# Optimization experiments

Measured on AMD Instinct MI355X. Metric: run time of the kernel, lower is better.

Reference implementation:

```python
import jax, jax.numpy as jnp
import numpy as np

# Mamba-1.4B-like dims
BATCH, SEQ, HID = 1, 2048, 2048
INTER, STATE, DT_RANK, KCONV = 4096, 16, 128, 4


def setup_inputs() -> dict:
    key = jax.random.key(0)
    ks = jax.random.split(key, 8)
    f = jnp.float32
    return {
        "input_states": jax.random.normal(ks[0], (BATCH, SEQ, HID), f),
        "in_proj_w": jax.random.normal(ks[1], (HID, 2 * INTER), f) * (HID ** -0.5),
        "conv_w": jax.random.normal(ks[2], (INTER, 1, KCONV), f) * (KCONV ** -0.5),  # (O, I/groups=1, K) depthwise
        "conv_b": jnp.zeros((INTER,), f),
        "x_proj_w": jax.random.normal(ks[3], (INTER, DT_RANK + 2 * STATE), f) * (INTER ** -0.5),
        "dt_proj_w": jax.random.normal(ks[4], (DT_RANK, INTER), f) * (DT_RANK ** -0.5),
        "dt_proj_b": jax.random.normal(ks[5], (INTER,), f) * 0.1,
        "A_log": jnp.log(jnp.broadcast_to(jnp.arange(1, STATE + 1, dtype=f), (INTER, STATE))),
        "D": jnp.ones((INTER,), f),
        "out_proj_w": jax.random.normal(ks[6], (INTER, HID), f) * (INTER ** -0.5),
    }


def _mamba_forward(input_states, in_proj_w, conv_w, conv_b, x_proj_w,
                   dt_proj_w, dt_proj_b, A_log, D, out_proj_w):
    Bsz, L, _ = input_states.shape
    Idim, _, K = conv_w.shape
    N = A_log.shape[1]
    R = dt_proj_w.shape[0]

    proj = input_states @ in_proj_w                       # (B, L, 2I)
    hidden, gate = jnp.split(proj, 2, axis=-1)            # each (B, L, I)

    # depthwise causal conv over sequence (pad K-1, keep first L outputs)
    xc = jnp.swapaxes(hidden, 1, 2)                       # (B, I, L)
    xc = jax.lax.conv_general_dilated(
        xc, conv_w, window_strides=(1,), padding=((K - 1, K - 1),),
        feature_group_count=Idim)
    xc = xc[:, :, :L] + conv_b[None, :, None]
    u = jax.nn.silu(jnp.swapaxes(xc, 1, 2))               # (B, L, I)

    # input-dependent SSM params
    ssm_in = u @ x_proj_w                                 # (B, L, R + 2N)
    dt_in, Bc, Cc = jnp.split(ssm_in, [R, R + N], axis=-1)
    dt = jax.nn.softplus(dt_in @ dt_proj_w + dt_proj_b)   # (B, L, I)
    A = -jnp.exp(A_log)                                   # (I, N)

    def step(state, xs):
        dt_t, B_t, C_t, u_t = xs                          # (B,I) (B,N) (B,N) (B,I)
        dA = jnp.exp(dt_t[:, :, None] * A[None])          # (B, I, N)
        state = state * dA + (dt_t * u_t)[:, :, None] * B_t[:, None, :]
        y_t = jnp.einsum('bin,bn->bi', state, C_t)
        return state, y_t

    xs = (jnp.swapaxes(dt, 0, 1), jnp.swapaxes(Bc, 0, 1),
          jnp.swapaxes(Cc, 0, 1), jnp.swapaxes(u, 0, 1))
    state0 = jnp.zeros((Bsz, Idim, N), dt.dtype)
    _, ys = jax.lax.scan(step, state0, xs)                # (L, B, I)
    y = jnp.swapaxes(ys, 0, 1)                            # (B, L, I)

    y = (y + u * D) * jax.nn.silu(gate)
    return y @ out_proj_w                                 # (B, L, H)


def reference(input_states, in_proj_w, conv_w, conv_b, x_proj_w,
              dt_proj_w, dt_proj_b, A_log, D, out_proj_w):
    return _mamba_forward(input_states, in_proj_w, conv_w, conv_b, x_proj_w,
                          dt_proj_w, dt_proj_b, A_log, D, out_proj_w)
```

## Files before the change

kernel.cpp:

```cpp
#include <hip/hip_runtime.h>
#include <stdint.h>

#define LSEQ 2048
#define HID  2048
#define IDIM 4096
#define NSTATE 16
#define RRANK 128
#define GDIM 160

#define GCHUNK 64
#define TCHUNK (LSEQ / GCHUNK)

typedef _Float16 f16x8 __attribute__((ext_vector_type(8)));
typedef _Float16 f16x2 __attribute__((ext_vector_type(2)));
typedef float f32x4 __attribute__((ext_vector_type(4)));

#define GLOAD_LDS16(g, l) __builtin_amdgcn_global_load_lds( \
    (const __attribute__((address_space(1))) void*)(g),     \
    (__attribute__((address_space(3))) void*)(l), 16, 0, 0)

__device__ __forceinline__ float softplus_f(float x) {
    if (x > 20.f) return x;
    return log1pf(__expf(x));
}
__device__ __forceinline__ float silu_f(float x) {
    return x / (1.f + __expf(-x));
}

__device__ __forceinline__ void transpose_tile(const float* __restrict__ in,
                                               _Float16* __restrict__ out,
                                               int R, int C, int tr, int tc,
                                               _Float16 (*tile)[66]) {
    const int c0 = tc * 64, r0 = tr * 64;
    const int t = threadIdx.x;
    const int tx = t & 15, ty = t >> 4;
    const int ox = t & 7, oy = t >> 3;
    const bool full = (c0 + 64 <= C) && (r0 + 64 <= R);
    if (full) {
        #pragma unroll
        for (int j = 0; j < 4; ++j) {
            int r = ty + j * 16;
            float4 v = *(const float4*)(in + (long)(r0 + r) * C + c0 + tx * 4);
            tile[r][tx * 4 + 0] = (_Float16)v.x;
            tile[r][tx * 4 + 1] = (_Float16)v.y;
            tile[r][tx * 4 + 2] = (_Float16)v.z;
            tile[r][tx * 4 + 3] = (_Float16)v.w;
        }
        __syncthreads();
        #pragma unroll
        for (int j = 0; j < 2; ++j) {
            int c = oy + j * 32;
            f16x8 v;
            #pragma unroll
            for (int e = 0; e < 8; ++e) v[e] = tile[ox * 8 + e][c];
            *(f16x8*)(out + (long)(c0 + c) * R + r0 + ox * 8) = v;
        }
    } else {
        #pragma unroll
        for (int j = 0; j < 4; ++j) {
            int r = ty + j * 16;
            #pragma unroll
            for (int e = 0; e < 4; ++e) {
                int c = c0 + tx * 4 + e;
                float v = (r0 + r < R && c < C) ? in[(long)(r0 + r) * C + c] : 0.f;
                tile[r][tx * 4 + e] = (_Float16)v;
            }
        }
        __syncthreads();
        #pragma unroll
        for (int j = 0; j < 2; ++j) {
            int c = c0 + oy + j * 32;
            if (c < C) {
                #pragma unroll
                for (int e = 0; e < 8; ++e) {
                    int r = r0 + ox * 8 + e;
                    if (r < R) out[(long)c * R + r] = tile[ox * 8 + e][oy + j * 32];
                }
            }
        }
    }
}

__global__ __launch_bounds__(256)
void prep_kernel(const float* __restrict__ x_in, const float* __restrict__ w_in,
                 _Float16* __restrict__ Xf, _Float16* __restrict__ Wt1) {
    __shared__ _Float16 tile[64][66];
    int b = blockIdx.x;
    if (b < 4096) { transpose_tile(w_in, Wt1, HID, 2 * IDIM, b / 128, b % 128, tile); return; }
    b -= 4096;
    long base = (long)b * 4096 + threadIdx.x * 16;
    #pragma unroll
    for (int h = 0; h < 2; ++h) {
        float4 a = *(const float4*)(x_in + base + h * 8);
        float4 c = *(const float4*)(x_in + base + h * 8 + 4);
        f16x8 v;
        v[0] = (_Float16)a.x; v[1] = (_Float16)a.y; v[2] = (_Float16)a.z; v[3] = (_Float16)a.w;
        v[4] = (_Float16)c.x; v[5] = (_Float16)c.y; v[6] = (_Float16)c.z; v[7] = (_Float16)c.w;
        *(f16x8*)(Xf + base + h * 8) = v;
    }
}

#define BM 128
#define BK 64

template <typename CT, bool SOFTPLUS>
__device__ __forceinline__
void gemm_core(const _Float16* __restrict__ A, const _Float16* __restrict__ Bt,
               CT* __restrict__ C, int M, int N, int K, int kc,
               const float* __restrict__ bias,
               _Float16* __restrict__ As, _Float16* __restrict__ Bs,
               int m0, int n0, int zz) {
    const int t = threadIdx.x;
    const int wave = t >> 6;
    const int lane = t & 63;
    const int wm = wave >> 1, wn = wave & 1;
    const int lrow = lane & 15;
    const int quad = lane >> 4;
    const int sw8 = (lrow & 7) * 8;

    f32x4 acc[4][4];
    #pragma unroll
    for (int mi = 0; mi < 4; ++mi)
        #pragma unroll
        for (int ni = 0; ni < 4; ++ni)
            #pragma unroll
            for (int r = 0; r < 4; ++r)
                acc[mi][ni][r] = 0.f;

    const int k_begin = zz * kc;
    const _Float16* pA[4];
    const _Float16* pB[4];
    #pragma unroll
    for (int j = 0; j < 4; ++j) {
        int s = j * 256 + t;
        int row = s >> 3;
        int ch = (s & 7) ^ (row & 7);
        pA[j] = A + (long)(m0 + row) * K + ch * 8 + k_begin;
        pB[j] = Bt + (long)(n0 + row) * K + ch * 8 + k_begin;
    }

    for (int kk = 0; kk < kc; kk += BK) {
        #pragma unroll
        for (int j = 0; j < 4; ++j) {
            GLOAD_LDS16(pA[j], As + (j * 256 + wave * 64) * 8);
            pA[j] += BK;
            GLOAD_LDS16(pB[j], Bs + (j * 256 + wave * 64) * 8);
            pB[j] += BK;
        }
        __syncthreads();

        #pragma unroll
        for (int h = 0; h < 2; ++h) {
            const int qoff = (h * 32 + quad * 8) ^ sw8;
            f16x8 af[4], bf[4];
            #pragma unroll
            for (int mi = 0; mi < 4; ++mi)
                af[mi] = *(const f16x8*)(As + (wm * 64 + mi * 16 + lrow) * BK + qoff);
            #pragma unroll
            for (int ni = 0; ni < 4; ++ni)
                bf[ni] = *(const f16x8*)(Bs + (wn * 64 + ni * 16 + lrow) * BK + qoff);
            #pragma unroll
            for (int mi = 0; mi < 4; ++mi)
                #pragma unroll
                for (int ni = 0; ni < 4; ++ni)
                    acc[mi][ni] = __builtin_amdgcn_mfma_f32_16x16x32_f16(af[mi], bf[ni], acc[mi][ni], 0, 0, 0);
        }
        __syncthreads();
    }

    CT* Cz = C + (long)zz * M * N;
    #pragma unroll
    for (int mi = 0; mi < 4; ++mi) {
        #pragma unroll
        for (int ni = 0; ni < 4; ++ni) {
            int col = n0 + wn * 64 + ni * 16 + lrow;
            if (col < N) {
                float bv = SOFTPLUS ? bias[col] : 0.f;
                #pragma unroll
                for (int r = 0; r < 4; ++r) {
                    int row = m0 + wm * 64 + mi * 16 + quad * 4 + r;
                    float v = acc[mi][ni][r];
                    if (SOFTPLUS) v = softplus_f(v + bv);
                    Cz[(long)row * N + col] = (CT)v;
                }
            }
        }
    }
}

template <typename CT, bool SOFTPLUS>
__global__ __launch_bounds__(256)
void gemm_bt_kernel(const _Float16* __restrict__ A, const _Float16* __restrict__ Bt,
                    CT* __restrict__ C, int M, int N, int K, int kc,
                    const float* __restrict__ bias) {
    __shared__ _Float16 As[BM * BK];
    __shared__ _Float16 Bs[128 * BK];
    gemm_core<CT, SOFTPLUS>(A, Bt, C, M, N, K, kc, bias, As, Bs,
                            blockIdx.y * BM, blockIdx.x * 128, blockIdx.z);
}

__global__ __launch_bounds__(256)
void inproj_plus_kernel(const _Float16* __restrict__ Xf, const _Float16* __restrict__ Wt1,
                        _Float16* __restrict__ proj,
                        const float* __restrict__ xw, const float* __restrict__ dtw,
                        const float* __restrict__ ow,
                        _Float16* __restrict__ Wt2, _Float16* __restrict__ Wt3,
                        _Float16* __restrict__ Wt4) {
    __shared__ _Float16 smem[BM * BK + 128 * BK];
    int b = blockIdx.x;
    if (b < 1024) {
        gemm_core<_Float16, false>(Xf, Wt1, proj, LSEQ, 2 * IDIM, HID, HID, nullptr,
                                   smem, smem + BM * BK, (b >> 6) * BM, (b & 63) * 128, 0);
        return;
    }
    b -= 1024;
    _Float16 (*tile)[66] = (_Float16 (*)[66])smem;
    if (b < 192) { transpose_tile(xw, Wt2, IDIM, GDIM, b / 3, b % 3, tile); return; }
    b -= 192;
    if (b < 128) { transpose_tile(dtw, Wt3, RRANK, IDIM, b / 64, b % 64, tile); return; }
    b -= 128;
    transpose_tile(ow, Wt4, IDIM, HID, b / 32, b % 32, tile);
}

__global__ void xproj_reduce_kernel(const float* __restrict__ part, float* __restrict__ ssm,
                                    _Float16* __restrict__ dtin) {
    int idx = blockIdx.x * 256 + threadIdx.x;
    if (idx >= LSEQ * GDIM) return;
    int t = idx / GDIM;
    int c = idx - t * GDIM;
    float v = 0.f;
    #pragma unroll
    for (int k = 0; k < 16; ++k)
        v += part[((long)k * LSEQ + t) * 256 + c];
    ssm[idx] = v;
    if (c < RRANK) dtin[t * RRANK + c] = (_Float16)v;
}

__global__ void opart_reduce_kernel(const _Float16* __restrict__ part, float* __restrict__ out) {
    long base = ((long)blockIdx.x * 256 + threadIdx.x) * 32;
    #pragma unroll
    for (int j = 0; j < 4; ++j) {
        f16x8 a = *(const f16x8*)(part + base + j * 8);
        f16x8 b = *(const f16x8*)(part + (long)LSEQ * HID + base + j * 8);
        float4 o0 = make_float4((float)a[0] + (float)b[0], (float)a[1] + (float)b[1],
                                (float)a[2] + (float)b[2], (float)a[3] + (float)b[3]);
        float4 o1 = make_float4((float)a[4] + (float)b[4], (float)a[5] + (float)b[5],
                                (float)a[6] + (float)b[6], (float)a[7] + (float)b[7]);
        *(float4*)(out + base + j * 8) = o0;
        *(float4*)(out + base + j * 8 + 4) = o1;
    }
}

__global__ void conv_silu_kernel(const _Float16* __restrict__ proj, const float* __restrict__ w,
                                 const float* __restrict__ b, _Float16* __restrict__ u16) {
    int idx = blockIdx.x * 256 + threadIdx.x;
    int i0 = (idx & 511) * 8;
    int t0 = (idx >> 9) * 4;
    f16x8 r[7];
    #pragma unroll
    for (int k = 0; k < 7; ++k) {
        int tt = t0 - 3 + k;
        if (tt >= 0) r[k] = *(const f16x8*)(proj + (long)tt * (2 * IDIM) + i0);
        else         r[k] = f16x8{0,0,0,0,0,0,0,0};
    }
    float4 wv[8]; float bb[8];
    #pragma unroll
    for (int j = 0; j < 8; ++j) { wv[j] = ((const float4*)w)[i0 + j]; bb[j] = b[i0 + j]; }
    #pragma unroll
    for (int tt = 0; tt < 4; ++tt) {
        f16x8 res;
        #pragma unroll
        for (int j = 0; j < 8; ++j) {
            float a = bb[j] + (float)r[tt][j] * wv[j].x + (float)r[tt+1][j] * wv[j].y
                            + (float)r[tt+2][j] * wv[j].z + (float)r[tt+3][j] * wv[j].w;
            res[j] = (_Float16)(a / (1.f + __expf(-a)));
        }
        *(f16x8*)(u16 + (long)(t0 + tt) * IDIM + i0) = res;
    }
}

__global__ __launch_bounds__(256)
void scan_pass1_kernel(const _Float16* __restrict__ dtf, const float* __restrict__ ssm,
                       const _Float16* __restrict__ u16, const float* __restrict__ A_log,
                       _Float16* __restrict__ Pc, _Float16* __restrict__ Sc) {
    const int c = blockIdx.y;
    const int i0 = (blockIdx.x * 256 + threadIdx.x) * 2;

    __shared__ float Bs[TCHUNK * 16];
    for (int idx = threadIdx.x; idx < TCHUNK * 16; idx += 256) {
        int t = idx >> 4, n = idx & 15;
        Bs[idx] = ssm[(c * TCHUNK + t) * GDIM + RRANK + n];
    }
    __syncthreads();

    float A[2][16];
    #pragma unroll
    for (int ch = 0; ch < 2; ++ch) {
        const float4* Ap = (const float4*)(A_log + (long)(i0 + ch) * 16);
        #pragma unroll
        for (int q = 0; q < 4; ++q) {
            float4 v = Ap[q];
            A[ch][q * 4 + 0] = -__expf(v.x);
            A[ch][q * 4 + 1] = -__expf(v.y);
            A[ch][q * 4 + 2] = -__expf(v.z);
            A[ch][q * 4 + 3] = -__expf(v.w);
        }
    }

    float s[2][16];
    float sumdt[2] = {0.f, 0.f};
    #pragma unroll
    for (int ch = 0; ch < 2; ++ch)
        #pragma unroll
        for (int n = 0; n < 16; ++n) s[ch][n] = 0.f;

    long base = (long)c * TCHUNK * IDIM + i0;
    for (int t = 0; t < TCHUNK; ++t) {
        f16x2 dt2 = *(const f16x2*)(dtf + base + (long)t * IDIM);
        f16x2 u2  = *(const f16x2*)(u16 + base + (long)t * IDIM);
        #pragma unroll
        for (int ch = 0; ch < 2; ++ch) {
            float dt = (float)dt2[ch];
            float dtu = dt * (float)u2[ch];
            sumdt[ch] += dt;
            #pragma unroll
            for (int n = 0; n < 16; ++n) {
                float dA = __expf(dt * A[ch][n]);
                s[ch][n] = s[ch][n] * dA + dtu * Bs[t * 16 + n];
            }
        }
    }

    long o = ((long)c * IDIM + i0) * 16;
    #pragma unroll
    for (int ch = 0; ch < 2; ++ch) {
        #pragma unroll
        for (int q = 0; q < 2; ++q) {
            f16x8 pv, sv;
            #pragma unroll
            for (int e = 0; e < 8; ++e) {
                pv[e] = (_Float16)__expf(A[ch][q * 8 + e] * sumdt[ch]);
                sv[e] = (_Float16)s[ch][q * 8 + e];
            }
            *(f16x8*)(Pc + o + ch * 16 + q * 8) = pv;
            *(f16x8*)(Sc + o + ch * 16 + q * 8) = sv;
        }
    }
}

__global__ void scan_combine_kernel(const _Float16* __restrict__ Pc, _Float16* __restrict__ ScInit) {
    int tid = blockIdx.x * 256 + threadIdx.x;
    const long stride = (long)IDIM * 16;
    const long off = (long)tid * 2;
    f16x2 p4[4], s4[4];
    #pragma unroll
    for (int k = 0; k < 4; ++k) {
        p4[k] = *(const f16x2*)(Pc + (long)k * stride + off);
        s4[k] = *(const f16x2*)(ScInit + (long)k * stride + off);
    }
    float c0 = 0.f, c1 = 0.f;
    for (int g = 0; g < GCHUNK / 4; ++g) {
        f16x2 pc[4], sc[4];
        #pragma unroll
        for (int k = 0; k < 4; ++k) { pc[k] = p4[k]; sc[k] = s4[k]; }
        if (g + 1 < GCHUNK / 4) {
            #pragma unroll
            for (int k = 0; k < 4; ++k) {
                long o2 = (long)((g + 1) * 4 + k) * stride + off;
                p4[k] = *(const f16x2*)(Pc + o2);
                s4[k] = *(const f16x2*)(ScInit + o2);
            }
        }
        #pragma unroll
        for (int k = 0; k < 4; ++k) {
            long o = (long)(g * 4 + k) * stride + off;
            *(f16x2*)(ScInit + o) = f16x2{(_Float16)c0, (_Float16)c1};
            c0 = c0 * (float)pc[k][0] + (float)sc[k][0];
            c1 = c1 * (float)pc[k][1] + (float)sc[k][1];
        }
    }
}

__global__ __launch_bounds__(256)
void scan_pass3_kernel(const _Float16* __restrict__ dtf, const float* __restrict__ ssm,
                       const _Float16* __restrict__ u16, const _Float16* __restrict__ proj,
                       const float* __restrict__ A_log, const float* __restrict__ Dp,
                       const _Float16* __restrict__ Init, _Float16* __restrict__ y16) {
    const int c = blockIdx.y;
    const int i0 = (blockIdx.x * 256 + threadIdx.x) * 2;

    __shared__ float Bs[TCHUNK * 16];
    __shared__ float Cs[TCHUNK * 16];
    for (int idx = threadIdx.x; idx < TCHUNK * 16; idx += 256) {
        int t = idx >> 4, n = idx & 15;
        Bs[idx] = ssm[(c * TCHUNK + t) * GDIM + RRANK + n];
        Cs[idx] = ssm[(c * TCHUNK + t) * GDIM + RRANK + NSTATE + n];
    }
    __syncthreads();

    float A[2][16];
    #pragma unroll
    for (int ch = 0; ch < 2; ++ch) {
        const float4* Ap = (const float4*)(A_log + (long)(i0 + ch) * 16);
        #pragma unroll
        for (int q = 0; q < 4; ++q) {
            float4 v = Ap[q];
            A[ch][q * 4 + 0] = -__expf(v.x);
            A[ch][q * 4 + 1] = -__expf(v.y);
            A[ch][q * 4 + 2] = -__expf(v.z);
            A[ch][q * 4 + 3] = -__expf(v.w);
        }
    }
    float2 Dv = *(const float2*)(Dp + i0);

    float s[2][16];
    {
        long o = ((long)c * IDIM + i0) * 16;
        #pragma unroll
        for (int ch = 0; ch < 2; ++ch)
            #pragma unroll
            for (int q = 0; q < 2; ++q) {
                f16x8 v = *(const f16x8*)(Init + o + ch * 16 + q * 8);
                #pragma unroll
                for (int e = 0; e < 8; ++e) s[ch][q * 8 + e] = (float)v[e];
            }
    }

    long base = (long)c * TCHUNK * IDIM + i0;
    for (int t = 0; t < TCHUNK; ++t) {
        f16x2 dt2 = *(const f16x2*)(dtf + base + (long)t * IDIM);
        f16x2 u2  = *(const f16x2*)(u16 + base + (long)t * IDIM);
        int tg = c * TCHUNK + t;
        f16x2 g2 = *(const f16x2*)(proj + (long)tg * (2 * IDIM) + IDIM + i0);
        f16x2 res;
        #pragma unroll
        for (int ch = 0; ch < 2; ++ch) {
            float dt = (float)dt2[ch];
            float uv = (float)u2[ch];
            float dtu = dt * uv;
            float y = 0.f;
            #pragma unroll
            for (int n = 0; n < 16; ++n) {
                float dA = __expf(dt * A[ch][n]);
                s[ch][n] = s[ch][n] * dA + dtu * Bs[t * 16 + n];
                y += s[ch][n] * Cs[t * 16 + n];
            }
            float g = (float)g2[ch];
            float Dch = ch ? Dv.y : Dv.x;
            res[ch] = (_Float16)((y + uv * Dch) * silu_f(g));
        }
        *(f16x2*)(y16 + base + (long)t * IDIM) = res;
    }
}

extern "C" void kernel_launch(void* const* d_in, const int* in_sizes, int n_in,
                              void* d_out, int out_size, void* d_ws, size_t ws_size,
                              hipStream_t stream) {
    const float* x_in  = (const float*)d_in[0];
    const float* w_in  = (const float*)d_in[1];
    const float* cw    = (const float*)d_in[2];
    const float* cb    = (const float*)d_in[3];
    const float* xw    = (const float*)d_in[4];
    const float* dtw   = (const float*)d_in[5];
    const float* dtb   = (const float*)d_in[6];
    const float* alog  = (const float*)d_in[7];
    const float* Dp    = (const float*)d_in[8];
    const float* ow    = (const float*)d_in[9];
    float* out = (float*)d_out;

    char* p = (char*)d_ws;
    auto alloc = [&](size_t bytes) { char* r = p; p += (bytes + 255) & ~255ull; return r; };
    _Float16* Xf    = (_Float16*)alloc((size_t)LSEQ * HID * 2);
    _Float16* Wt1   = (_Float16*)alloc((size_t)2 * IDIM * HID * 2);
    _Float16* proj  = (_Float16*)alloc((size_t)LSEQ * 2 * IDIM * 2);
    _Float16* u16   = (_Float16*)alloc((size_t)LSEQ * IDIM * 2);
    _Float16* Wt2   = (_Float16*)alloc((size_t)256 * IDIM * 2);
    float*    ssm   = (float*)alloc((size_t)LSEQ * GDIM * 4);
    _Float16* dtin  = (_Float16*)alloc((size_t)LSEQ * RRANK * 2);
    _Float16* Wt3   = (_Float16*)alloc((size_t)IDIM * RRANK * 2);
    _Float16* dtf   = (_Float16*)alloc((size_t)LSEQ * IDIM * 2);
    _Float16* Wt4   = (_Float16*)alloc((size_t)HID * IDIM * 2);
    _Float16* y16   = (_Float16*)alloc((size_t)LSEQ * IDIM * 2);

    float* xpart = (float*)Wt1;
    _Float16* Pc = (_Float16*)Wt1;
    _Float16* Sc = Pc + (size_t)GCHUNK * IDIM * 16;
    _Float16* opart = (_Float16*)Wt1;

    prep_kernel<<<5120, 256, 0, stream>>>(x_in, w_in, Xf, Wt1);
    inproj_plus_kernel<<<1024 + 192 + 128 + 2048, 256, 0, stream>>>(
        Xf, Wt1, proj, xw, dtw, ow, Wt2, Wt3, Wt4);
    conv_silu_kernel<<<(LSEQ / 4) * (IDIM / 8) / 256, 256, 0, stream>>>(proj, cw, cb, u16);
    gemm_bt_kernel<float, false><<<dim3(2, LSEQ / BM, 16), 256, 0, stream>>>(
        u16, Wt2, xpart, LSEQ, 256, IDIM, IDIM / 16, nullptr);
    xproj_reduce_kernel<<<(LSEQ * GDIM + 255) / 256, 256, 0, stream>>>(xpart, ssm, dtin);
    gemm_bt_kernel<_Float16, true><<<dim3(IDIM / 128, LSEQ / BM, 1), 256, 0, stream>>>(
        dtin, Wt3, dtf, LSEQ, IDIM, RRANK, RRANK, dtb);
    scan_pass1_kernel<<<dim3(IDIM / 512, GCHUNK), 256, 0, stream>>>(
        dtf, ssm, u16, alog, Pc, Sc);
    scan_combine_kernel<<<(IDIM * NSTATE / 2) / 256, 256, 0, stream>>>(Pc, Sc);
    scan_pass3_kernel<<<dim3(IDIM / 512, GCHUNK), 256, 0, stream>>>(
        dtf, ssm, u16, proj, alog, Dp, Sc, y16);
    gemm_bt_kernel<_Float16, false><<<dim3(HID / 128, LSEQ / BM, 2), 256, 0, stream>>>(
        y16, Wt4, opart, LSEQ, HID, IDIM, IDIM / 2, nullptr);
    opart_reduce_kernel<<<(LSEQ * HID / 32) / 256, 256, 0, stream>>>(opart, out);
}
```

Before: 460.5 us.

## Use 256x256 multi-stage LDS-DMA GEMM for in_proj and out_proj

Adds a 512-thread GEMM core with 256x256 output tiles, a 4-slot async global-to-LDS pipeline, XOR-swizzled LDS layout and XCD-aware block remapping. It is used for the in-projection and for the out-projection, which now runs as a 4-way split-K with fp32 partials followed by a 4-input reduction. Weight transposes are packed two per 512-thread block. Larger tiles and deeper prefetch are meant to raise MFMA utilization and data reuse, at the cost of 128KB of LDS per block, heavier register use, and more partial-sum traffic in the out-projection.

```diff
diff --git a/kernel.cpp b/kernel.cpp
--- a/kernel.cpp
+++ b/kernel.cpp
@@ -30,9 +30,8 @@
 __device__ __forceinline__ void transpose_tile(const float* __restrict__ in,
                                                _Float16* __restrict__ out,
                                                int R, int C, int tr, int tc,
-                                               _Float16 (*tile)[66]) {
+                                               _Float16 (*tile)[66], int t) {
     const int c0 = tc * 64, r0 = tr * 64;
-    const int t = threadIdx.x;
     const int tx = t & 15, ty = t >> 4;
     const int ox = t & 7, oy = t >> 3;
     const bool full = (c0 + 64 <= C) && (r0 + 64 <= R);
@@ -86,7 +85,7 @@
                  _Float16* __restrict__ Xf, _Float16* __restrict__ Wt1) {
     __shared__ _Float16 tile[64][66];
     int b = blockIdx.x;
-    if (b < 4096) { transpose_tile(w_in, Wt1, HID, 2 * IDIM, b / 128, b % 128, tile); return; }
+    if (b < 4096) { transpose_tile(w_in, Wt1, HID, 2 * IDIM, b / 128, b % 128, tile, threadIdx.x); return; }
     b -= 4096;
     long base = (long)b * 4096 + threadIdx.x * 16;
     #pragma unroll
@@ -199,27 +198,142 @@
                             blockIdx.y * BM, blockIdx.x * 128, blockIdx.z);
 }
 
-__global__ __launch_bounds__(256)
+template <typename CT>
+__device__ __forceinline__
+void gemm256_core(const _Float16* __restrict__ A, const _Float16* __restrict__ Bt,
+                  CT* __restrict__ C, int M, int N, int K, int kc,
+                  int m0, int n0, int zz, _Float16* __restrict__ sm) {
+    const int t = threadIdx.x;
+    const int wave = t >> 6, lane = t & 63;
+    const int wm = wave >> 2, wn = wave & 3;
+    const int lrow = lane & 15, quad = lane >> 4;
+    const int ns = kc >> 5;
+
+    const int rA = t >> 2;
+    const int qe = (((t & 3) ^ (rA & 3)) * 8);
+    const _Float16* gA0 = A  + (size_t)(m0 + rA) * K + (size_t)zz * kc + qe;
+    const _Float16* gA1 = gA0 + (size_t)128 * K;
+    const _Float16* gB0 = Bt + (size_t)(n0 + rA) * K + (size_t)zz * kc + qe;
+    const _Float16* gB1 = gB0 + (size_t)128 * K;
+
+    _Float16* const bsm = sm + 32768;
+    const int dA = wave * 512;
+
+    f32x4 acc[8][4];
+    #pragma unroll
+    for (int mi = 0; mi < 8; ++mi)
+        #pragma unroll
+        for (int ni = 0; ni < 4; ++ni)
+            #pragma unroll
+            for (int r = 0; r < 4; ++r) acc[mi][ni][r] = 0.f;
+
+    #define ISSUE_SLICE(slot) do {                                          \
+        _Float16* as_ = sm  + (slot) * 8192;                                \
+        _Float16* bs_ = bsm + (slot) * 8192;                                \
+        GLOAD_LDS16(gA0, as_ + dA);                                         \
+        GLOAD_LDS16(gA1, as_ + 4096 + dA);                                  \
+        GLOAD_LDS16(gB0, bs_ + dA);                                         \
+        GLOAD_LDS16(gB1, bs_ + 4096 + dA);                                  \
+        gA0 += 32; gA1 += 32; gB0 += 32; gB1 += 32;                         \
+    } while (0)
+
+    ISSUE_SLICE(0); ISSUE_SLICE(1); ISSUE_SLICE(2);
+    asm volatile("s_waitcnt vmcnt(8)" ::: "memory");
+    __builtin_amdgcn_s_barrier();
+    __builtin_amdgcn_sched_barrier(0);
+
+    const int arow0 = (wm * 128 + lrow) * 32;
+    const int brow0 = (wn * 64 + lrow) * 32;
+    const int koff  = ((quad ^ (lrow & 3)) * 8);
+
+    for (int s2 = 0; s2 < ns; ++s2) {
+        const _Float16* as_ = sm  + (s2 & 3) * 8192;
+        const _Float16* bs_ = bsm + (s2 & 3) * 8192;
+        if (s2 + 3 < ns) ISSUE_SLICE((s2 + 3) & 3);
+        __builtin_amdgcn_sched_barrier(0);
+
+        f16x8 af[8], bf[4];
+        #pragma unroll
+        for (int mi = 0; mi < 8; ++mi)
+            af[mi] = *(const f16x8*)(as_ + arow0 + mi * 512 + koff);
+        #pragma unroll
+        for (int ni = 0; ni < 4; ++ni)
+            bf[ni] = *(const f16x8*)(bs_ + brow0 + ni * 512 + koff);
+
+        __builtin_amdgcn_s_setprio(1);
+        #pragma unroll
+        for (int mi = 0; mi < 8; ++mi)
+            #pragma unroll
+            for (int ni = 0; ni < 4; ++ni)
+                acc[mi][ni] = __builtin_amdgcn_mfma_f32_16x16x32_f16(af[mi], bf[ni], acc[mi][ni], 0, 0, 0);
+        __builtin_amdgcn_s_setprio(0);
+
+        if (s2 + 1 < ns) {
+            if (s2 + 4 <= ns)      asm volatile("s_waitcnt vmcnt(8)" ::: "memory");
+            else if (s2 + 3 == ns) asm volatile("s_waitcnt vmcnt(4)" ::: "memory");
+            else                   asm volatile("s_waitcnt vmcnt(0)" ::: "memory");
+            __builtin_amdgcn_s_barrier();
+            __builtin_amdgcn_sched_barrier(0);
+        }
+    }
+    #undef ISSUE_SLICE
+
+    CT* Cz = C + (size_t)zz * ((size_t)M * N);
+    const int crow = m0 + wm * 128 + quad * 4;
+    const int ccol = n0 + wn * 64 + lrow;
+    #pragma unroll
+    for (int mi = 0; mi < 8; ++mi)
+        #pragma unroll
+        for (int ni = 0; ni < 4; ++ni)
+            #pragma unroll
+            for (int r = 0; r < 4; ++r)
+                Cz[(size_t)(crow + mi * 16 + r) * N + ccol + ni * 16] = (CT)acc[mi][ni][r];
+}
+
+__global__ __launch_bounds__(512, 2)
+void gemm256_kernel(const _Float16* __restrict__ A, const _Float16* __restrict__ Bt,
+                    float* __restrict__ C, int M, int N, int K, int kc) {
+    __shared__ _Float16 sm[65536];
+    int nb = gridDim.x * gridDim.y * gridDim.z;
+    int f0 = blockIdx.x + gridDim.x * (blockIdx.y + gridDim.y * blockIdx.z);
+    int cpx = nb >> 3;
+    int f = (f0 & 7) * cpx + (f0 >> 3);
+    int bx = f % gridDim.x;
+    int r2 = f / gridDim.x;
+    int by = r2 % gridDim.y;
+    int bz = r2 / gridDim.y;
+    gemm256_core<float>(A, Bt, C, M, N, K, kc, by * 256, bx * 256, bz, sm);
+}
+
+__global__ __launch_bounds__(512, 2)
 void inproj_plus_kernel(const _Float16* __restrict__ Xf, const _Float16* __restrict__ Wt1,
                         _Float16* __restrict__ proj,
                         const float* __restrict__ xw, const float* __restrict__ dtw,
                         const float* __restrict__ ow,
                         _Float16* __restrict__ Wt2, _Float16* __restrict__ Wt3,
                         _Float16* __restrict__ Wt4) {
-    __shared__ _Float16 smem[BM * BK + 128 * BK];
+    __shared__ _Float16 sm[65536];
     int b = blockIdx.x;
-    if (b < 1024) {
-        gemm_core<_Float16, false>(Xf, Wt1, proj, LSEQ, 2 * IDIM, HID, HID, nullptr,
-                                   smem, smem + BM * BK, (b >> 6) * BM, (b & 63) * 128, 0);
+    if (b < 256) {
+        int f = (b & 7) * 32 + (b >> 3);
+        gemm256_core<_Float16>(Xf, Wt1, proj, LSEQ, 2 * IDIM, HID, HID,
+                               (f >> 5) * 256, (f & 31) * 256, 0, sm);
         return;
     }
-    b -= 1024;
-    _Float16 (*tile)[66] = (_Float16 (*)[66])smem;
-    if (b < 192) { transpose_tile(xw, Wt2, IDIM, GDIM, b / 3, b % 3, tile); return; }
-    b -= 192;
-    if (b < 128) { transpose_tile(dtw, Wt3, RRANK, IDIM, b / 64, b % 64, tile); return; }
-    b -= 128;
-    transpose_tile(ow, Wt4, IDIM, HID, b / 32, b % 32, tile);
+    b -= 256;
+    const int half = threadIdx.x >> 8;
+    const int tid  = threadIdx.x & 255;
+    int tile_idx = b * 2 + half;
+    _Float16 (*tile)[66] = (_Float16 (*)[66])(sm + half * 4224);
+    if (tile_idx < 192) {
+        transpose_tile(xw, Wt2, IDIM, GDIM, tile_idx / 3, tile_idx % 3, tile, tid);
+    } else if (tile_idx < 320) {
+        int j = tile_idx - 192;
+        transpose_tile(dtw, Wt3, RRANK, IDIM, j / 64, j % 64, tile, tid);
+    } else {
+        int j = tile_idx - 320;
+        transpose_tile(ow, Wt4, IDIM, HID, j / 32, j % 32, tile, tid);
+    }
 }
 
 __global__ void xproj_reduce_kernel(const float* __restrict__ part, float* __restrict__ ssm,
@@ -236,18 +350,20 @@
     if (c < RRANK) dtin[t * RRANK + c] = (_Float16)v;
 }
 
-__global__ void opart_reduce_kernel(const _Float16* __restrict__ part, float* __restrict__ out) {
-    long base = ((long)blockIdx.x * 256 + threadIdx.x) * 32;
-    #pragma unroll
-    for (int j = 0; j < 4; ++j) {
-        f16x8 a = *(const f16x8*)(part + base + j * 8);
-        f16x8 b = *(const f16x8*)(part + (long)LSEQ * HID + base + j * 8);
-        float4 o0 = make_float4((float)a[0] + (float)b[0], (float)a[1] + (float)b[1],
-                                (float)a[2] + (float)b[2], (float)a[3] + (float)b[3]);
-        float4 o1 = make_float4((float)a[4] + (float)b[4], (float)a[5] + (float)b[5],
-                                (float)a[6] + (float)b[6], (float)a[7] + (float)b[7]);
-        *(float4*)(out + base + j * 8) = o0;
-        *(float4*)(out + base + j * 8 + 4) = o1;
+__global__ void opart_reduce_kernel(const float* __restrict__ part, float* __restrict__ out) {
+    size_t base = ((size_t)blockIdx.x * 256 + threadIdx.x) * 32;
+    const size_t SL = (size_t)LSEQ * HID;
+    #pragma unroll
+    for (int j = 0; j < 8; ++j) {
+        float4 a = *(const float4*)(part + base + j * 4);
+        float4 b = *(const float4*)(part + SL + base + j * 4);
+        float4 c = *(const float4*)(part + 2 * SL + base + j * 4);
+        float4 d = *(const float4*)(part + 3 * SL + base + j * 4);
+        float4 o = make_float4(a.x + b.x + c.x + d.x,
+                               a.y + b.y + c.y + d.y,
+                               a.z + b.z + c.z + d.z,
+                               a.w + b.w + c.w + d.w);
+        *(float4*)(out + base + j * 4) = o;
     }
 }
 
@@ -485,10 +601,10 @@
     float* xpart = (float*)Wt1;
     _Float16* Pc = (_Float16*)Wt1;
     _Float16* Sc = Pc + (size_t)GCHUNK * IDIM * 16;
-    _Float16* opart = (_Float16*)Wt1;
+    float* opart32 = (float*)proj;
 
     prep_kernel<<<5120, 256, 0, stream>>>(x_in, w_in, Xf, Wt1);
-    inproj_plus_kernel<<<1024 + 192 + 128 + 2048, 256, 0, stream>>>(
+    inproj_plus_kernel<<<256 + 1184, 512, 0, stream>>>(
         Xf, Wt1, proj, xw, dtw, ow, Wt2, Wt3, Wt4);
     conv_silu_kernel<<<(LSEQ / 4) * (IDIM / 8) / 256, 256, 0, stream>>>(proj, cw, cb, u16);
     gemm_bt_kernel<float, false><<<dim3(2, LSEQ / BM, 16), 256, 0, stream>>>(
@@ -501,7 +617,7 @@
     scan_combine_kernel<<<(IDIM * NSTATE / 2) / 256, 256, 0, stream>>>(Pc, Sc);
     scan_pass3_kernel<<<dim3(IDIM / 512, GCHUNK), 256, 0, stream>>>(
         dtf, ssm, u16, proj, alog, Dp, Sc, y16);
-    gemm_bt_kernel<_Float16, false><<<dim3(HID / 128, LSEQ / BM, 2), 256, 0, stream>>>(
-        y16, Wt4, opart, LSEQ, HID, IDIM, IDIM / 2, nullptr);
-    opart_reduce_kernel<<<(LSEQ * HID / 32) / 256, 256, 0, stream>>>(opart, out);
-}
+    gemm256_kernel<<<dim3(HID / 256, LSEQ / 256, 4), 512, 0, stream>>>(
+        y16, Wt4, opart32, LSEQ, HID, IDIM, IDIM / 4);
+    opart_reduce_kernel<<<(LSEQ * HID / 32) / 256, 256, 0, stream>>>(opart32, out);
+}
```

After: 473.7 us. 2.9% more time.
